# Kernel tuning notes

Hardware: AMD Instinct MI355X
Metric: run time of the kernel (lower is better)

Reference implementation:

```python
import jax, jax.numpy as jnp
import numpy as np

B, CIN, H, W = 2, 3, 768, 768
CB = 32          # backbone out_channels (= channels_mid for heads)
ORDER = 5
MARGIN = 3.0     # ScaledTanh margin of refinement head


def _conv(x, w, b, pad):
    # x: [N,C,H,W], w: [O,I,kh,kw]
    y = jax.lax.conv_general_dilated(x, w, (1, 1), [(pad, pad), (pad, pad)],
                                     dimension_numbers=('NCHW', 'OIHW', 'NCHW'))
    return y + b[None, :, None, None]


def _readout(x, w1, b1, s, t, w2, b2, pad):
    # conv(k) -> batchnorm(eval, folded to scale/shift) -> relu -> dropout(eval=id) -> conv1x1
    h = _conv(x, w1, b1, pad)
    h = jax.nn.relu(h * s[None, :, None, None] + t[None, :, None, None])
    return _conv(h, w2, b2, 0)


def setup_inputs() -> dict:
    key = jax.random.key(0)
    ks = iter(jax.random.split(key, 16))
    def rn(shape, scale=0.05):
        return jax.random.normal(next(ks), shape, jnp.float32) * scale
    d = {'inputs': jax.random.normal(next(ks), (B, CIN, H, W), jnp.float32)}
    d['bb_w'] = rn((CB, CIN, 3, 3)); d['bb_b'] = jnp.zeros((CB,), jnp.float32)
    def head(name, k, cout):
        d[name + '_w1'] = rn((CB, CB, k, k)); d[name + '_b1'] = jnp.zeros((CB,), jnp.float32)
        d[name + '_s'] = jnp.ones((CB,), jnp.float32); d[name + '_t'] = jnp.zeros((CB,), jnp.float32)
        d[name + '_w2'] = rn((cout, CB, 1, 1)); d[name + '_b2'] = jnp.zeros((cout,), jnp.float32)
    head('score', 3, 2)
    head('loc', 7, 2)
    head('four', 7, ORDER * 4)
    head('ref', 7, 2)
    return d


def reference(inputs, bb_w, bb_b,
              score_w1, score_b1, score_s, score_t, score_w2, score_b2,
              loc_w1, loc_b1, loc_s, loc_t, loc_w2, loc_b2,
              four_w1, four_b1, four_s, four_t, four_w2, four_b2,
              ref_w1, ref_b1, ref_s, ref_t, ref_w2, ref_b2):
    # backbone (simple conv + relu; out_channels is an int so contour == refinement features)
    feats = jax.nn.relu(_conv(inputs, bb_w, bb_b, 1))
    scores = _readout(feats, score_w1, score_b1, score_s, score_t, score_w2, score_b2, 1)
    locations = _readout(feats, loc_w1, loc_b1, loc_s, loc_t, loc_w2, loc_b2, 3)
    fourier = _readout(feats, four_w1, four_b1, four_s, four_t, four_w2, four_b2, 3)
    # ReadOut final activation ScaledTanh(3.0), then CPNCore multiplies by internal margin 1.0;
    # feature HW == input HW (stride 1), so F.interpolate is a no-op.
    refinement = jnp.tanh(_readout(feats, ref_w1, ref_b1, ref_s, ref_t, ref_w2, ref_b2, 3)) * MARGIN
    return (scores, locations, refinement, fourier)
```

## Files before the change

kernel.cpp:

```cpp
#include <hip/hip_runtime.h>
#include <hip/hip_bf16.h>
#include <cmath>

#define HH 768
#define WW 768
#define HWSZ (768*768)

typedef __attribute__((ext_vector_type(8))) short bhalf8;
typedef __attribute__((ext_vector_type(4))) float f32x4;
typedef __attribute__((ext_vector_type(16))) float f32x16;

__device__ inline ushort f2bf(float f) {
  __hip_bfloat16 h = __float2bfloat16(f);
  return *reinterpret_cast<ushort*>(&h);
}

__global__ __launch_bounds__(256) void wxform_kernel(
    const float* __restrict__ w1, const float* __restrict__ b1,
    const float* __restrict__ s,  const float* __restrict__ t,
    ushort* __restrict__ wT, float* __restrict__ bb, int npos)
{
  int i = blockIdx.x * 256 + threadIdx.x;
  if (i < npos * 1024) {
    int pos = i >> 10, mc = i & 1023, m = mc >> 5, c = mc & 31;
    wT[i] = f2bf(w1[(m * 32 + c) * npos + pos] * s[m]);
  }
  if (i < 32) bb[i] = b1[i] * s[i] + t[i];
}

__global__ __launch_bounds__(256) void backbone_kernel(
    const float* __restrict__ x, const float* __restrict__ w,
    const float* __restrict__ bias, ushort* __restrict__ feats)
{
  int p = blockIdx.x * 256 + threadIdx.x;
  int bb  = p / HWSZ;
  int rem = p - bb * HWSZ;
  int y   = rem / WW;
  int xx  = rem - y * WW;
  const float* xb = x + (size_t)bb * 3 * HWSZ;

  float v[3][3][3];
  #pragma unroll
  for (int c = 0; c < 3; c++)
    #pragma unroll
    for (int dy = 0; dy < 3; dy++)
      #pragma unroll
      for (int dx = 0; dx < 3; dx++) {
        int yy = y + dy - 1, xq = xx + dx - 1;
        v[c][dy][dx] = (yy >= 0 && yy < HH && xq >= 0 && xq < WW)
                         ? xb[(size_t)c * HWSZ + yy * WW + xq] : 0.f;
      }

  union { ushort u[32]; uint4 q[4]; } pk;
  #pragma unroll
  for (int o = 0; o < 32; o++) {
    float acc = bias[o];
    #pragma unroll
    for (int c = 0; c < 3; c++)
      #pragma unroll
      for (int dy = 0; dy < 3; dy++)
        #pragma unroll
        for (int dx = 0; dx < 3; dx++)
          acc = fmaf(w[((o * 3 + c) * 3 + dy) * 3 + dx], v[c][dy][dx], acc);
    pk.u[o] = f2bf(fmaxf(acc, 0.f));
  }
  uint4* dst = (uint4*)(feats + ((size_t)bb * HWSZ + rem) * 32);
  #pragma unroll
  for (int i = 0; i < 4; i++) dst[i] = pk.q[i];
}

template <int COUT, bool DO_TANH>
__device__ inline void head_epilogue(
    const f32x16 acc[2], const float* __restrict__ bbh,
    const float* __restrict__ w2, const float* __restrict__ b2,
    float* __restrict__ out_base, float* mid,
    int wv, int qr, int qc, int kg, int by, int bx, int bb)
{
  #pragma unroll
  for (int n = 0; n < 2; n++) {
    int pix = (wv * 4 + 2 * n + qr) * 16 + qc;
    #pragma unroll
    for (int rg = 0; rg < 4; rg++) {
      int m0 = 8 * rg + 4 * kg;
      f32x4 v;
      #pragma unroll
      for (int j = 0; j < 4; j++)
        v[j] = fmaxf(acc[n][rg * 4 + j] + bbh[m0 + j], 0.f);
      *(f32x4*)(mid + pix * 36 + m0) = v;
    }
  }
  __syncthreads();

  int t = threadIdx.x;
  float mv[32];
  #pragma unroll
  for (int j2 = 0; j2 < 8; j2++)
    *(f32x4*)(mv + 4 * j2) = *(const f32x4*)(mid + t * 36 + 4 * j2);

  int oy = by * 16 + (t >> 4), ox = bx * 16 + (t & 15);
  size_t opix = (size_t)oy * WW + ox;
  float* ob = out_base + (size_t)bb * COUT * HWSZ;
  #pragma unroll
  for (int oc = 0; oc < COUT; oc++) {
    float a2 = b2[oc];
    #pragma unroll
    for (int m = 0; m < 32; m++) a2 = fmaf(w2[oc * 32 + m], mv[m], a2);
    if (DO_TANH) a2 = tanhf(a2) * 3.0f;
    ob[(size_t)oc * HWSZ + opix] = a2;
  }
  __syncthreads();
}

template <bool GATE1, int COUT0, bool TANH0, int COUT1, bool TANH1>
__global__ __launch_bounds__(256, 2) void heads2_kernel(
    const ushort* __restrict__ feats,
    const ushort* __restrict__ wt0, const ushort* __restrict__ wt1,
    const float*  __restrict__ bbh0, const float* __restrict__ bbh1,
    const float* __restrict__ w20, const float* __restrict__ b20,
    const float* __restrict__ w21, const float* __restrict__ b21,
    float* __restrict__ out0, float* __restrict__ out1)
{
  constexpr int TW = 22, CPAD = 40;
  __shared__ __align__(16) char smem[TW * TW * CPAD * 2];
  ushort* tile = (ushort*)smem;

  int bx = blockIdx.x % 48;
  int by = (blockIdx.x / 48) % 48;
  int bb = blockIdx.x / 2304;
  int x0 = bx * 16 - 3, y0 = by * 16 - 3;
  const ushort* fB = feats + (size_t)bb * HWSZ * 32;

  for (int p = threadIdx.x; p < TW * TW; p += 256) {
    int py = p / TW, pxx = p % TW;
    int yy = y0 + py, xx = x0 + pxx;
    uint4 q0 = {0,0,0,0}, q1 = {0,0,0,0}, q2 = {0,0,0,0}, q3 = {0,0,0,0};
    if (yy >= 0 && yy < HH && xx >= 0 && xx < WW) {
      const uint4* src = (const uint4*)(fB + ((size_t)yy * WW + xx) * 32);
      q0 = src[0]; q1 = src[1]; q2 = src[2]; q3 = src[3];
    }
    uint4* dst = (uint4*)(tile + (size_t)p * CPAD);
    dst[0] = q0; dst[1] = q1; dst[2] = q2; dst[3] = q3;
  }
  __syncthreads();

  int l  = threadIdx.x & 63;
  int wv = threadIdx.x >> 6;
  int q  = l & 31;
  int kg = l >> 5;
  int qr = q >> 4, qc = q & 15;

  const ushort* pb = tile + ((wv * 4 + qr) * TW + qc) * CPAD + kg * 8;
  const int aoff = q * 32 + kg * 8;

  f32x16 acc0[2] = {};
  f32x16 acc1[2] = {};

  #pragma unroll
  for (int ky = 0; ky < 7; ky++) {
    #pragma unroll
    for (int kx = 0; kx < 7; kx++) {
      const int tap = ky * 7 + kx;
      const bool act1 = !GATE1 || (ky >= 2 && ky <= 4 && kx >= 2 && kx <= 4);
      const int tap1 = GATE1 ? (ky - 2) * 3 + (kx - 2) : tap;

      bhalf8 a0[2], a1[2];
      #pragma unroll
      for (int kh = 0; kh < 2; kh++)
        a0[kh] = *(const bhalf8*)(wt0 + tap * 1024 + aoff + kh * 16);
      if (act1)
        #pragma unroll
        for (int kh = 0; kh < 2; kh++)
          a1[kh] = *(const bhalf8*)(wt1 + tap1 * 1024 + aoff + kh * 16);

      bhalf8 bfr[2][2];
      #pragma unroll
      for (int n = 0; n < 2; n++)
        #pragma unroll
        for (int kh = 0; kh < 2; kh++)
          bfr[n][kh] = *(const bhalf8*)(pb + (ky * TW + kx) * CPAD
                                           + n * 2 * TW * CPAD + kh * 16);

      #pragma unroll
      for (int n = 0; n < 2; n++)
        #pragma unroll
        for (int kh = 0; kh < 2; kh++) {
          acc0[n] = __builtin_amdgcn_mfma_f32_32x32x16_bf16(a0[kh], bfr[n][kh], acc0[n], 0, 0, 0);
          if (act1)
            acc1[n] = __builtin_amdgcn_mfma_f32_32x32x16_bf16(a1[kh], bfr[n][kh], acc1[n], 0, 0, 0);
        }
    }
  }

  __syncthreads();
  float* mid = (float*)smem;

  head_epilogue<COUT0, TANH0>(acc0, bbh0, w20, b20, out0, mid, wv, qr, qc, kg, by, bx, bb);
  head_epilogue<COUT1, TANH1>(acc1, bbh1, w21, b21, out1, mid, wv, qr, qc, kg, by, bx, bb);
}

extern "C" void kernel_launch(void* const* d_in, const int* in_sizes, int n_in,
                              void* d_out, int out_size, void* d_ws, size_t ws_size,
                              hipStream_t stream) {
  const float* input = (const float*)d_in[0];
  const float* bb_w  = (const float*)d_in[1];
  const float* bb_b  = (const float*)d_in[2];

  ushort* feats = (ushort*)d_ws;
  char* base = (char*)d_ws;
  const size_t FEATS_BYTES = (size_t)2 * HWSZ * 32 * 2;
  const size_t WT_STRIDE   = 49 * 1024 * 2;
  ushort* wT0 = (ushort*)(base + FEATS_BYTES);
  float*  bb0 = (float*)(base + FEATS_BYTES + 4 * WT_STRIDE);
  (void)out_size; (void)ws_size; (void)n_in; (void)in_sizes;

  float* out = (float*)d_out;
  float* outS = out;
  float* outL = out + (size_t)4  * HWSZ;
  float* outR = out + (size_t)8  * HWSZ;
  float* outF = out + (size_t)12 * HWSZ;

  const int npos_h[4] = {9, 49, 49, 49};
  for (int h = 0; h < 4; h++) {
    const float* w1 = (const float*)d_in[3 + h * 6 + 0];
    const float* b1 = (const float*)d_in[3 + h * 6 + 1];
    const float* s  = (const float*)d_in[3 + h * 6 + 2];
    const float* t  = (const float*)d_in[3 + h * 6 + 3];
    ushort* wT = (ushort*)((char*)wT0 + h * WT_STRIDE);
    float*  bbv = bb0 + h * 32;
    int n = npos_h[h] * 1024;
    wxform_kernel<<<(n + 255) / 256, 256, 0, stream>>>(w1, b1, s, t, wT, bbv, npos_h[h]);
  }

  backbone_kernel<<<4608, 256, 0, stream>>>(input, bb_w, bb_b, feats);

  const ushort* wtS = (const ushort*)((char*)wT0 + 0 * WT_STRIDE);
  const ushort* wtL = (const ushort*)((char*)wT0 + 1 * WT_STRIDE);
  const ushort* wtF = (const ushort*)((char*)wT0 + 2 * WT_STRIDE);
  const ushort* wtR = (const ushort*)((char*)wT0 + 3 * WT_STRIDE);

  heads2_kernel<false, 2, false, 20, false><<<2 * 48 * 48, 256, 0, stream>>>(
      feats, wtL, wtF, bb0 + 32, bb0 + 64,
      (const float*)d_in[13], (const float*)d_in[14],
      (const float*)d_in[19], (const float*)d_in[20],
      outL, outF);

  heads2_kernel<true, 2, true, 2, false><<<2 * 48 * 48, 256, 0, stream>>>(
      feats, wtR, wtS, bb0 + 96, bb0 + 0,
      (const float*)d_in[25], (const float*)d_in[26],
      (const float*)d_in[7],  (const float*)d_in[8],
      outR, outS);
}
```

Before: 490.0 us.

## Widen head tile to 16x32 pixels with row-wise MFMA fragments and bf16 mid buffer

Each block now computes a 16x32 output tile instead of 16x16. Each wave covers four full 32-pixel rows, so the weight fragments loaded per tap are reused across four MFMA column groups instead of two, and the halo overhead per output pixel shrinks. The intermediate activations are stored in LDS as bf16 instead of fp32 so the 512-pixel epilogue buffer fits in the larger feature tile. In exchange, accumulator registers per thread double (up to 128 VGPRs of accumulators), which may hurt occupancy or cause spills. The extra bf16 rounding of the mid activations also adds precision loss.

```diff
diff --git a/kernel.cpp b/kernel.cpp
--- a/kernel.cpp
+++ b/kernel.cpp
@@ -13,6 +13,9 @@
 __device__ inline ushort f2bf(float f) {
   __hip_bfloat16 h = __float2bfloat16(f);
   return *reinterpret_cast<ushort*>(&h);
+}
+__device__ inline float bf2f(ushort u) {
+  union { unsigned int i; float f; } v; v.i = ((unsigned int)u) << 16; return v.f;
 }
 
 __global__ __launch_bounds__(256) void wxform_kernel(
@@ -71,42 +74,53 @@
 
 template <int COUT, bool DO_TANH>
 __device__ inline void head_epilogue(
-    const f32x16 acc[2], const float* __restrict__ bbh,
+    const f32x16 acc[4], const float* __restrict__ bbh,
     const float* __restrict__ w2, const float* __restrict__ b2,
-    float* __restrict__ out_base, float* mid,
-    int wv, int qr, int qc, int kg, int by, int bx, int bb)
-{
-  #pragma unroll
-  for (int n = 0; n < 2; n++) {
-    int pix = (wv * 4 + 2 * n + qr) * 16 + qc;
-    #pragma unroll
-    for (int rg = 0; rg < 4; rg++) {
-      int m0 = 8 * rg + 4 * kg;
-      f32x4 v;
-      #pragma unroll
-      for (int j = 0; j < 4; j++)
-        v[j] = fmaxf(acc[n][rg * 4 + j] + bbh[m0 + j], 0.f);
-      *(f32x4*)(mid + pix * 36 + m0) = v;
+    float* __restrict__ out_base, ushort* mid,
+    int wv, int q, int kg, int by, int bx, int bb)
+{
+  #pragma unroll
+  for (int n = 0; n < 4; n++) {
+    int pix = (wv * 4 + n) * 32 + q;
+    #pragma unroll
+    for (int rq = 0; rq < 4; rq++) {
+      int m0 = 8 * rq + 4 * kg;
+      ushort u[4];
+      #pragma unroll
+      for (int rr = 0; rr < 4; rr++)
+        u[rr] = f2bf(fmaxf(acc[n][rq * 4 + rr] + bbh[m0 + rr], 0.f));
+      uint2 pkv;
+      pkv.x = (unsigned int)u[0] | ((unsigned int)u[1] << 16);
+      pkv.y = (unsigned int)u[2] | ((unsigned int)u[3] << 16);
+      *(uint2*)(mid + pix * 36 + m0) = pkv;
     }
   }
   __syncthreads();
 
   int t = threadIdx.x;
-  float mv[32];
-  #pragma unroll
-  for (int j2 = 0; j2 < 8; j2++)
-    *(f32x4*)(mv + 4 * j2) = *(const f32x4*)(mid + t * 36 + 4 * j2);
-
-  int oy = by * 16 + (t >> 4), ox = bx * 16 + (t & 15);
-  size_t opix = (size_t)oy * WW + ox;
-  float* ob = out_base + (size_t)bb * COUT * HWSZ;
-  #pragma unroll
-  for (int oc = 0; oc < COUT; oc++) {
-    float a2 = b2[oc];
-    #pragma unroll
-    for (int m = 0; m < 32; m++) a2 = fmaf(w2[oc * 32 + m], mv[m], a2);
-    if (DO_TANH) a2 = tanhf(a2) * 3.0f;
-    ob[(size_t)oc * HWSZ + opix] = a2;
+  #pragma unroll
+  for (int rep = 0; rep < 2; rep++) {
+    int pix = t + rep * 256;
+    float mv[32];
+    #pragma unroll
+    for (int j = 0; j < 8; j++) {
+      uint2 r = *(const uint2*)(mid + pix * 36 + j * 4);
+      mv[j * 4 + 0] = bf2f((ushort)(r.x & 0xffff));
+      mv[j * 4 + 1] = bf2f((ushort)(r.x >> 16));
+      mv[j * 4 + 2] = bf2f((ushort)(r.y & 0xffff));
+      mv[j * 4 + 3] = bf2f((ushort)(r.y >> 16));
+    }
+    int oy = by * 16 + (pix >> 5), ox = bx * 32 + (pix & 31);
+    size_t opix = (size_t)oy * WW + ox;
+    float* ob = out_base + (size_t)bb * COUT * HWSZ;
+    #pragma unroll
+    for (int oc = 0; oc < COUT; oc++) {
+      float a2 = b2[oc];
+      #pragma unroll
+      for (int m = 0; m < 32; m++) a2 = fmaf(w2[oc * 32 + m], mv[m], a2);
+      if (DO_TANH) a2 = tanhf(a2) * 3.0f;
+      ob[(size_t)oc * HWSZ + opix] = a2;
+    }
   }
   __syncthreads();
 }
@@ -120,40 +134,38 @@
     const float* __restrict__ w21, const float* __restrict__ b21,
     float* __restrict__ out0, float* __restrict__ out1)
 {
-  constexpr int TW = 22, CPAD = 40;
-  __shared__ __align__(16) char smem[TW * TW * CPAD * 2];
-  ushort* tile = (ushort*)smem;
-
-  int bx = blockIdx.x % 48;
-  int by = (blockIdx.x / 48) % 48;
-  int bb = blockIdx.x / 2304;
-  int x0 = bx * 16 - 3, y0 = by * 16 - 3;
+  constexpr int TR = 22, TC = 38, CPAD = 40;
+  __shared__ __align__(16) ushort smem[TR * TC * CPAD];
+
+  int bx = blockIdx.x % 24;
+  int by = (blockIdx.x / 24) % 48;
+  int bb = blockIdx.x / 1152;
+  int x0 = bx * 32 - 3, y0 = by * 16 - 3;
   const ushort* fB = feats + (size_t)bb * HWSZ * 32;
 
-  for (int p = threadIdx.x; p < TW * TW; p += 256) {
-    int py = p / TW, pxx = p % TW;
-    int yy = y0 + py, xx = x0 + pxx;
+  for (int p = threadIdx.x; p < TR * TC; p += 256) {
+    int r = p / TC, cl = p - r * TC;
+    int yy = y0 + r, xx = x0 + cl;
     uint4 q0 = {0,0,0,0}, q1 = {0,0,0,0}, q2 = {0,0,0,0}, q3 = {0,0,0,0};
     if (yy >= 0 && yy < HH && xx >= 0 && xx < WW) {
       const uint4* src = (const uint4*)(fB + ((size_t)yy * WW + xx) * 32);
       q0 = src[0]; q1 = src[1]; q2 = src[2]; q3 = src[3];
     }
-    uint4* dst = (uint4*)(tile + (size_t)p * CPAD);
+    uint4* dst = (uint4*)(smem + (size_t)p * CPAD);
     dst[0] = q0; dst[1] = q1; dst[2] = q2; dst[3] = q3;
   }
   __syncthreads();
 
-  int l  = threadIdx.x & 63;
-  int wv = threadIdx.x >> 6;
-  int q  = l & 31;
-  int kg = l >> 5;
-  int qr = q >> 4, qc = q & 15;
-
-  const ushort* pb = tile + ((wv * 4 + qr) * TW + qc) * CPAD + kg * 8;
+  const int l  = threadIdx.x & 63;
+  const int wv = threadIdx.x >> 6;
+  const int q  = l & 31;
+  const int kg = l >> 5;
+
+  const ushort* pb = smem + ((wv * 4) * TC + q) * CPAD + kg * 8;
   const int aoff = q * 32 + kg * 8;
 
-  f32x16 acc0[2] = {};
-  f32x16 acc1[2] = {};
+  f32x16 acc0[4] = {};
+  f32x16 acc1[4] = {};
 
   #pragma unroll
   for (int ky = 0; ky < 7; ky++) {
@@ -172,30 +184,26 @@
         for (int kh = 0; kh < 2; kh++)
           a1[kh] = *(const bhalf8*)(wt1 + tap1 * 1024 + aoff + kh * 16);
 
-      bhalf8 bfr[2][2];
-      #pragma unroll
-      for (int n = 0; n < 2; n++)
-        #pragma unroll
-        for (int kh = 0; kh < 2; kh++)
-          bfr[n][kh] = *(const bhalf8*)(pb + (ky * TW + kx) * CPAD
-                                           + n * 2 * TW * CPAD + kh * 16);
-
-      #pragma unroll
-      for (int n = 0; n < 2; n++)
-        #pragma unroll
-        for (int kh = 0; kh < 2; kh++) {
-          acc0[n] = __builtin_amdgcn_mfma_f32_32x32x16_bf16(a0[kh], bfr[n][kh], acc0[n], 0, 0, 0);
-          if (act1)
-            acc1[n] = __builtin_amdgcn_mfma_f32_32x32x16_bf16(a1[kh], bfr[n][kh], acc1[n], 0, 0, 0);
+      #pragma unroll
+      for (int n = 0; n < 4; n++) {
+        const ushort* bp = pb + ((n + ky) * TC + kx) * CPAD;
+        bhalf8 b0 = *(const bhalf8*)(bp);
+        bhalf8 b1 = *(const bhalf8*)(bp + 16);
+        acc0[n] = __builtin_amdgcn_mfma_f32_32x32x16_bf16(a0[0], b0, acc0[n], 0, 0, 0);
+        acc0[n] = __builtin_amdgcn_mfma_f32_32x32x16_bf16(a0[1], b1, acc0[n], 0, 0, 0);
+        if (act1) {
+          acc1[n] = __builtin_amdgcn_mfma_f32_32x32x16_bf16(a1[0], b0, acc1[n], 0, 0, 0);
+          acc1[n] = __builtin_amdgcn_mfma_f32_32x32x16_bf16(a1[1], b1, acc1[n], 0, 0, 0);
         }
-    }
-  }
-
-  __syncthreads();
-  float* mid = (float*)smem;
-
-  head_epilogue<COUT0, TANH0>(acc0, bbh0, w20, b20, out0, mid, wv, qr, qc, kg, by, bx, bb);
-  head_epilogue<COUT1, TANH1>(acc1, bbh1, w21, b21, out1, mid, wv, qr, qc, kg, by, bx, bb);
+      }
+    }
+  }
+
+  __syncthreads();
+  ushort* mid = smem;
+
+  head_epilogue<COUT0, TANH0>(acc0, bbh0, w20, b20, out0, mid, wv, q, kg, by, bx, bb);
+  head_epilogue<COUT1, TANH1>(acc1, bbh1, w21, b21, out1, mid, wv, q, kg, by, bx, bb);
 }
 
 extern "C" void kernel_launch(void* const* d_in, const int* in_sizes, int n_in,
@@ -238,13 +246,15 @@
   const ushort* wtF = (const ushort*)((char*)wT0 + 2 * WT_STRIDE);
   const ushort* wtR = (const ushort*)((char*)wT0 + 3 * WT_STRIDE);
 
-  heads2_kernel<false, 2, false, 20, false><<<2 * 48 * 48, 256, 0, stream>>>(
+  const int GRID = 2 * 48 * 24;
+
+  heads2_kernel<false, 2, false, 20, false><<<GRID, 256, 0, stream>>>(
       feats, wtL, wtF, bb0 + 32, bb0 + 64,
       (const float*)d_in[13], (const float*)d_in[14],
       (const float*)d_in[19], (const float*)d_in[20],
       outL, outF);
 
-  heads2_kernel<true, 2, true, 2, false><<<2 * 48 * 48, 256, 0, stream>>>(
+  heads2_kernel<true, 2, true, 2, false><<<GRID, 256, 0, stream>>>(
       feats, wtR, wtS, bb0 + 96, bb0 + 0,
       (const float*)d_in[25], (const float*)d_in[26],
       (const float*)d_in[7],  (const float*)d_in[8],
```

After: 870.5 us. +77.7%, slower.

## Fuse three 7x7 heads into one kernel and split score head out

Applied to the files above, without the earlier changes.

The two paired-head kernels become one kernel that computes the loc, fourier and refinement 7x7 convolutions from a single shared feature tile, plus a separate small kernel for the 3x3 score head. Previously the 22x22 halo tile was loaded twice and the score head sat under the 7x7 loop with gated taps. The fused kernel carries three accumulator pairs, which raises register pressure under launch bounds of two blocks per SM and risks spills or lower occupancy. The score kernel uses a smaller tile and requests four blocks per SM.

```diff
diff --git a/kernel.cpp b/kernel.cpp
--- a/kernel.cpp
+++ b/kernel.cpp
@@ -111,14 +111,16 @@
   __syncthreads();
 }
 
-template <bool GATE1, int COUT0, bool TANH0, int COUT1, bool TANH1>
-__global__ __launch_bounds__(256, 2) void heads2_kernel(
+__global__ __launch_bounds__(256, 2) void heads3_kernel(
     const ushort* __restrict__ feats,
-    const ushort* __restrict__ wt0, const ushort* __restrict__ wt1,
-    const float*  __restrict__ bbh0, const float* __restrict__ bbh1,
-    const float* __restrict__ w20, const float* __restrict__ b20,
-    const float* __restrict__ w21, const float* __restrict__ b21,
-    float* __restrict__ out0, float* __restrict__ out1)
+    const ushort* __restrict__ wtL, const ushort* __restrict__ wtF,
+    const ushort* __restrict__ wtR,
+    const float* __restrict__ bbL, const float* __restrict__ bbF,
+    const float* __restrict__ bbR,
+    const float* __restrict__ w2L, const float* __restrict__ b2L,
+    const float* __restrict__ w2F, const float* __restrict__ b2F,
+    const float* __restrict__ w2R, const float* __restrict__ b2R,
+    float* __restrict__ outL, float* __restrict__ outF, float* __restrict__ outR)
 {
   constexpr int TW = 22, CPAD = 40;
   __shared__ __align__(16) char smem[TW * TW * CPAD * 2];
@@ -152,25 +154,23 @@
   const ushort* pb = tile + ((wv * 4 + qr) * TW + qc) * CPAD + kg * 8;
   const int aoff = q * 32 + kg * 8;
 
-  f32x16 acc0[2] = {};
-  f32x16 acc1[2] = {};
+  f32x16 accL[2] = {};
+  f32x16 accF[2] = {};
+  f32x16 accR[2] = {};
 
   #pragma unroll
   for (int ky = 0; ky < 7; ky++) {
     #pragma unroll
     for (int kx = 0; kx < 7; kx++) {
       const int tap = ky * 7 + kx;
-      const bool act1 = !GATE1 || (ky >= 2 && ky <= 4 && kx >= 2 && kx <= 4);
-      const int tap1 = GATE1 ? (ky - 2) * 3 + (kx - 2) : tap;
-
-      bhalf8 a0[2], a1[2];
-      #pragma unroll
-      for (int kh = 0; kh < 2; kh++)
-        a0[kh] = *(const bhalf8*)(wt0 + tap * 1024 + aoff + kh * 16);
-      if (act1)
-        #pragma unroll
-        for (int kh = 0; kh < 2; kh++)
-          a1[kh] = *(const bhalf8*)(wt1 + tap1 * 1024 + aoff + kh * 16);
+
+      bhalf8 aL[2], aF[2], aR[2];
+      #pragma unroll
+      for (int kh = 0; kh < 2; kh++) {
+        aL[kh] = *(const bhalf8*)(wtL + tap * 1024 + aoff + kh * 16);
+        aF[kh] = *(const bhalf8*)(wtF + tap * 1024 + aoff + kh * 16);
+        aR[kh] = *(const bhalf8*)(wtR + tap * 1024 + aoff + kh * 16);
+      }
 
       bhalf8 bfr[2][2];
       #pragma unroll
@@ -184,9 +184,9 @@
       for (int n = 0; n < 2; n++)
         #pragma unroll
         for (int kh = 0; kh < 2; kh++) {
-          acc0[n] = __builtin_amdgcn_mfma_f32_32x32x16_bf16(a0[kh], bfr[n][kh], acc0[n], 0, 0, 0);
-          if (act1)
-            acc1[n] = __builtin_amdgcn_mfma_f32_32x32x16_bf16(a1[kh], bfr[n][kh], acc1[n], 0, 0, 0);
+          accL[n] = __builtin_amdgcn_mfma_f32_32x32x16_bf16(aL[kh], bfr[n][kh], accL[n], 0, 0, 0);
+          accF[n] = __builtin_amdgcn_mfma_f32_32x32x16_bf16(aF[kh], bfr[n][kh], accF[n], 0, 0, 0);
+          accR[n] = __builtin_amdgcn_mfma_f32_32x32x16_bf16(aR[kh], bfr[n][kh], accR[n], 0, 0, 0);
         }
     }
   }
@@ -194,8 +194,76 @@
   __syncthreads();
   float* mid = (float*)smem;
 
-  head_epilogue<COUT0, TANH0>(acc0, bbh0, w20, b20, out0, mid, wv, qr, qc, kg, by, bx, bb);
-  head_epilogue<COUT1, TANH1>(acc1, bbh1, w21, b21, out1, mid, wv, qr, qc, kg, by, bx, bb);
+  head_epilogue<2,  false>(accL, bbL, w2L, b2L, outL, mid, wv, qr, qc, kg, by, bx, bb);
+  head_epilogue<20, false>(accF, bbF, w2F, b2F, outF, mid, wv, qr, qc, kg, by, bx, bb);
+  head_epilogue<2,  true >(accR, bbR, w2R, b2R, outR, mid, wv, qr, qc, kg, by, bx, bb);
+}
+
+__global__ __launch_bounds__(256, 4) void score_kernel(
+    const ushort* __restrict__ feats,
+    const ushort* __restrict__ wtS, const float* __restrict__ bbS,
+    const float* __restrict__ w2S, const float* __restrict__ b2S,
+    float* __restrict__ outS)
+{
+  constexpr int TW = 18, CPAD = 40;
+  constexpr int SMEM_BYTES = 256 * 36 * 4;
+  __shared__ __align__(16) char smem[SMEM_BYTES];
+  ushort* tile = (ushort*)smem;
+
+  int bx = blockIdx.x % 48;
+  int by = (blockIdx.x / 48) % 48;
+  int bb = blockIdx.x / 2304;
+  int x0 = bx * 16 - 1, y0 = by * 16 - 1;
+  const ushort* fB = feats + (size_t)bb * HWSZ * 32;
+
+  for (int p = threadIdx.x; p < TW * TW; p += 256) {
+    int py = p / TW, pxx = p % TW;
+    int yy = y0 + py, xx = x0 + pxx;
+    uint4 q0 = {0,0,0,0}, q1 = {0,0,0,0}, q2 = {0,0,0,0}, q3 = {0,0,0,0};
+    if (yy >= 0 && yy < HH && xx >= 0 && xx < WW) {
+      const uint4* src = (const uint4*)(fB + ((size_t)yy * WW + xx) * 32);
+      q0 = src[0]; q1 = src[1]; q2 = src[2]; q3 = src[3];
+    }
+    uint4* dst = (uint4*)(tile + (size_t)p * CPAD);
+    dst[0] = q0; dst[1] = q1; dst[2] = q2; dst[3] = q3;
+  }
+  __syncthreads();
+
+  int l  = threadIdx.x & 63;
+  int wv = threadIdx.x >> 6;
+  int q  = l & 31;
+  int kg = l >> 5;
+  int qr = q >> 4, qc = q & 15;
+
+  const ushort* pb = tile + ((wv * 4 + qr) * TW + qc) * CPAD + kg * 8;
+  const int aoff = q * 32 + kg * 8;
+
+  f32x16 acc[2] = {};
+
+  #pragma unroll
+  for (int ky = 0; ky < 3; ky++) {
+    #pragma unroll
+    for (int kx = 0; kx < 3; kx++) {
+      const int tap = ky * 3 + kx;
+      bhalf8 a0[2];
+      #pragma unroll
+      for (int kh = 0; kh < 2; kh++)
+        a0[kh] = *(const bhalf8*)(wtS + tap * 1024 + aoff + kh * 16);
+      #pragma unroll
+      for (int n = 0; n < 2; n++) {
+        #pragma unroll
+        for (int kh = 0; kh < 2; kh++) {
+          bhalf8 bf = *(const bhalf8*)(pb + (ky * TW + kx) * CPAD
+                                          + n * 2 * TW * CPAD + kh * 16);
+          acc[n] = __builtin_amdgcn_mfma_f32_32x32x16_bf16(a0[kh], bf, acc[n], 0, 0, 0);
+        }
+      }
+    }
+  }
+
+  __syncthreads();
+  float* mid = (float*)smem;
+  head_epilogue<2, false>(acc, bbS, w2S, b2S, outS, mid, wv, qr, qc, kg, by, bx, bb);
 }
 
 extern "C" void kernel_launch(void* const* d_in, const int* in_sizes, int n_in,
@@ -238,15 +306,17 @@
   const ushort* wtF = (const ushort*)((char*)wT0 + 2 * WT_STRIDE);
   const ushort* wtR = (const ushort*)((char*)wT0 + 3 * WT_STRIDE);
 
-  heads2_kernel<false, 2, false, 20, false><<<2 * 48 * 48, 256, 0, stream>>>(
-      feats, wtL, wtF, bb0 + 32, bb0 + 64,
+  const int GRID = 2 * 48 * 48;
+
+  heads3_kernel<<<GRID, 256, 0, stream>>>(
+      feats, wtL, wtF, wtR,
+      bb0 + 32, bb0 + 64, bb0 + 96,
       (const float*)d_in[13], (const float*)d_in[14],
       (const float*)d_in[19], (const float*)d_in[20],
-      outL, outF);
-
-  heads2_kernel<true, 2, true, 2, false><<<2 * 48 * 48, 256, 0, stream>>>(
-      feats, wtR, wtS, bb0 + 96, bb0 + 0,
       (const float*)d_in[25], (const float*)d_in[26],
-      (const float*)d_in[7],  (const float*)d_in[8],
-      outR, outS);
-}
+      outL, outF, outR);
+
+  score_kernel<<<GRID, 256, 0, stream>>>(
+      feats, wtS, bb0 + 0,
+      (const float*)d_in[7], (const float*)d_in[8], outS);
+}
```

Result: slower. 501.4 us (+2.3%).
